# Kernel tuning notes

Measured on AMD Instinct MI355X. Metric: run time of the kernel, lower is better.

Reference implementation:

```python
import jax, jax.numpy as jnp
import numpy as np

DIM = 1024
B, S = 4, 2048


def setup_inputs() -> dict:
    key = jax.random.key(0)
    kx, kq, kk, kv, ko = jax.random.split(key, 5)
    scale = 1.0 / np.sqrt(DIM)
    return {
        "x": jax.random.normal(kx, (B, S, DIM), dtype=jnp.float32),
        "wq": jax.random.normal(kq, (DIM, DIM), dtype=jnp.float32) * scale,
        "wk": jax.random.normal(kk, (DIM, DIM), dtype=jnp.float32) * scale,
        "wv": jax.random.normal(kv, (DIM, DIM), dtype=jnp.float32) * scale,
        "wo": jax.random.normal(ko, (DIM, DIM), dtype=jnp.float32) * scale,
    }


def reference(x, wq, wk, wv, wo):
    # nn.Linear(y) = y @ W.T ; weights stored [out, in]
    q = jnp.einsum("bsd,ed->bse", x, wq)
    k = jnp.einsum("bsd,ed->bse", x, wk)
    v = jnp.einsum("bsd,ed->bse", x, wv)
    # NOTE: no head split in original module; full-dim attention, scale = sqrt(dim)
    scores = jnp.einsum("bqd,bkd->bqk", q, k) / jnp.sqrt(jnp.float32(DIM))
    attn = jax.nn.softmax(scores, axis=-1)
    ctx = jnp.einsum("bqk,bkd->bqd", attn, v)
    return jnp.einsum("bsd,ed->bse", ctx, wo)
```

## Files before the change

### kernel.cpp

```cpp
#include <hip/hip_runtime.h>
#include <hip/hip_bf16.h>
#include <cstdio>
#include <cstdint>


typedef __attribute__((ext_vector_type(8))) short short8;
typedef __attribute__((ext_vector_type(4))) float f32x4;

#define AS1(p) ((const __attribute__((address_space(1))) void*)(p))
#define AS3(p) ((__attribute__((address_space(3))) void*)(p))

__device__ __forceinline__ unsigned short f2bf(float f) {
  union { float f; uint32_t u; } c; c.f = f;
  uint32_t u = c.u + 0x7fffu + ((c.u >> 16) & 1u);
  return (unsigned short)(u >> 16);
}

__global__ void cvt_f32_bf16(const float* __restrict__ in,
                             unsigned short* __restrict__ out, int n4) {
  int i = blockIdx.x * 256 + threadIdx.x;
  if (i >= n4) return;
  float4 v = ((const float4*)in)[i];
  ushort4 o;
  o.x = f2bf(v.x); o.y = f2bf(v.y); o.z = f2bf(v.z); o.w = f2bf(v.w);
  ((ushort4*)out)[i] = o;
}

__global__ void transpose_bf16(const unsigned short* __restrict__ V,
                               unsigned short* __restrict__ Vt) {
  __shared__ unsigned short tile[64][72];
  const int b = blockIdx.z;
  const unsigned short* v = V + (size_t)b * 2048 * 1024;
  unsigned short* vt = Vt + (size_t)b * 1024 * 2048;
  const int d0 = blockIdx.x * 64, s0 = blockIdx.y * 64;
  const int t = threadIdx.x;
#pragma unroll
  for (int it = 0; it < 16; ++it) {
    int idx = it * 256 + t, r = idx >> 6, c = idx & 63;
    tile[r][c] = v[(size_t)(s0 + r) * 1024 + d0 + c];
  }
  __syncthreads();
#pragma unroll
  for (int it = 0; it < 16; ++it) {
    int idx = it * 256 + t, r = idx >> 6, c = idx & 63;
    vt[(size_t)(d0 + r) * 2048 + s0 + c] = tile[c][r];
  }
}

__global__ void softmax_rows(const float* __restrict__ S,
                             unsigned short* __restrict__ P) {
  const size_t row = blockIdx.x;
  const float* s = S + row * 2048;
  const int t = threadIdx.x, l = t & 63, w = t >> 6;
  float4 v0 = ((const float4*)s)[t * 2];
  float4 v1 = ((const float4*)s)[t * 2 + 1];
  float x[8] = {v0.x, v0.y, v0.z, v0.w, v1.x, v1.y, v1.z, v1.w};
  float m = x[0];
#pragma unroll
  for (int j = 1; j < 8; ++j) m = fmaxf(m, x[j]);
#pragma unroll
  for (int d = 32; d; d >>= 1) m = fmaxf(m, __shfl_xor(m, d));
  __shared__ float rm[4], rs[4];
  if (l == 0) rm[w] = m;
  __syncthreads();
  m = fmaxf(fmaxf(rm[0], rm[1]), fmaxf(rm[2], rm[3]));
  float e[8], sum = 0.f;
#pragma unroll
  for (int j = 0; j < 8; ++j) { e[j] = __expf(x[j] - m); sum += e[j]; }
#pragma unroll
  for (int d = 32; d; d >>= 1) sum += __shfl_xor(sum, d);
  if (l == 0) rs[w] = sum;
  __syncthreads();
  float inv = 1.0f / (rs[0] + rs[1] + rs[2] + rs[3]);
  short8 o;
#pragma unroll
  for (int j = 0; j < 8; ++j) o[j] = (short)f2bf(e[j] * inv);
  *(short8*)(P + row * 2048 + t * 8) = o;
}

__device__ __forceinline__ void store_out(float* p, float v) { *p = v; }
__device__ __forceinline__ void store_out(unsigned short* p, float v) { *p = f2bf(v); }

template <typename OutT>
__global__ __launch_bounds__(256, 2) void gemm_bt(
    const unsigned short* __restrict__ A, const unsigned short* __restrict__ B,
    OutT* __restrict__ C, int lda, int ldb, int ldc, int kIters,
    long long aStride, long long bStride, long long cStride, float scale) {
  __shared__ unsigned short ldsA[4096];
  __shared__ unsigned short ldsB[4096];
  const int t = threadIdx.x, l = t & 63, w = t >> 6;
  const int wr = w >> 1, wc = w & 1;
  const int r0 = blockIdx.y * 128, c0 = blockIdx.x * 128;
  A += (size_t)blockIdx.z * aStride;
  B += (size_t)blockIdx.z * bStride;
  C += (size_t)blockIdx.z * cStride;

  const unsigned short* aP = A + (size_t)(r0 + w * 16 + (l & 15)) * lda + (l >> 4) * 8;
  const unsigned short* bP = B + (size_t)(c0 + w * 16 + (l & 15)) * ldb + (l >> 4) * 8;
  const size_t a64 = (size_t)64 * lda, b64 = (size_t)64 * ldb;
  unsigned short* dA1 = &ldsA[w * 512];
  unsigned short* dA2 = &ldsA[2048 + w * 512];
  unsigned short* dB1 = &ldsB[w * 512];
  unsigned short* dB2 = &ldsB[2048 + w * 512];

  f32x4 acc[4][4] = {};

  for (int kt = 0; kt < kIters; ++kt) {
    __builtin_amdgcn_global_load_lds(AS1(aP),       AS3(dA1), 16, 0, 0);
    __builtin_amdgcn_global_load_lds(AS1(aP + a64), AS3(dA2), 16, 0, 0);
    __builtin_amdgcn_global_load_lds(AS1(bP),       AS3(dB1), 16, 0, 0);
    __builtin_amdgcn_global_load_lds(AS1(bP + b64), AS3(dB2), 16, 0, 0);
    aP += 32; bP += 32;
    __syncthreads();
    short8 af[4], bfv[4];
#pragma unroll
    for (int m = 0; m < 4; ++m)
      af[m] = *(const short8*)&ldsA[(wr * 4 + m) * 512 + l * 8];
#pragma unroll
    for (int n = 0; n < 4; ++n)
      bfv[n] = *(const short8*)&ldsB[(wc * 4 + n) * 512 + l * 8];
#pragma unroll
    for (int m = 0; m < 4; ++m)
#pragma unroll
      for (int n = 0; n < 4; ++n)
        acc[m][n] = __builtin_amdgcn_mfma_f32_16x16x32_bf16(af[m], bfv[n], acc[m][n], 0, 0, 0);
    __syncthreads();
  }

  const int cr = (l >> 4) * 4, cc = l & 15;
#pragma unroll
  for (int m = 0; m < 4; ++m)
#pragma unroll
    for (int n = 0; n < 4; ++n) {
      int col = c0 + wc * 64 + n * 16 + cc;
#pragma unroll
      for (int i = 0; i < 4; ++i) {
        int row = r0 + wr * 64 + m * 16 + cr + i;
        store_out(&C[(size_t)row * ldc + col], acc[m][n][i] * scale);
      }
    }
}

static const size_t OFF_XB  = 0;
static const size_t OFF_WQ  = 16777216;
static const size_t OFF_WK  = 18874368;
static const size_t OFF_WV  = 20971520;
static const size_t OFF_WO  = 23068672;
static const size_t OFF_Q   = 25165824;
static const size_t OFF_K   = 41943040;
static const size_t OFF_V   = 58720256;
static const size_t OFF_VT  = 75497472;
static const size_t OFF_SC  = 92274688;
static const size_t OFF_P   = 159383552;
static const size_t OFF_CTX = 192937984;
static const size_t WS_NEED = 209715200;

extern "C" void kernel_launch(void* const* d_in, const int* in_sizes, int n_in,
                              void* d_out, int out_size, void* d_ws, size_t ws_size,
                              hipStream_t stream) {
  const float* x  = (const float*)d_in[0];
  const float* wq = (const float*)d_in[1];
  const float* wk = (const float*)d_in[2];
  const float* wv = (const float*)d_in[3];
  const float* wo = (const float*)d_in[4];
  float* out = (float*)d_out;

  if (ws_size < WS_NEED) {
    fprintf(stderr, "kernel_launch: ws_size=%zu < needed %zu\n", ws_size, WS_NEED);
    return;
  }
  char* ws = (char*)d_ws;
  unsigned short* xb  = (unsigned short*)(ws + OFF_XB);
  unsigned short* wqb = (unsigned short*)(ws + OFF_WQ);
  unsigned short* wkb = (unsigned short*)(ws + OFF_WK);
  unsigned short* wvb = (unsigned short*)(ws + OFF_WV);
  unsigned short* wob = (unsigned short*)(ws + OFF_WO);
  unsigned short* Qb  = (unsigned short*)(ws + OFF_Q);
  unsigned short* Kb  = (unsigned short*)(ws + OFF_K);
  unsigned short* Vb  = (unsigned short*)(ws + OFF_V);
  unsigned short* Vt  = (unsigned short*)(ws + OFF_VT);
  float*          Sc  = (float*)(ws + OFF_SC);
  unsigned short* Pb  = (unsigned short*)(ws + OFF_P);
  unsigned short* Cx  = (unsigned short*)(ws + OFF_CTX);

  cvt_f32_bf16<<<8192, 256, 0, stream>>>(x,  xb,  2097152);
  cvt_f32_bf16<<<1024, 256, 0, stream>>>(wq, wqb, 262144);
  cvt_f32_bf16<<<1024, 256, 0, stream>>>(wk, wkb, 262144);
  cvt_f32_bf16<<<1024, 256, 0, stream>>>(wv, wvb, 262144);
  cvt_f32_bf16<<<1024, 256, 0, stream>>>(wo, wob, 262144);

  gemm_bt<unsigned short><<<dim3(8, 64, 1), 256, 0, stream>>>(
      xb, wqb, Qb, 1024, 1024, 1024, 32, 0, 0, 0, 1.0f);
  gemm_bt<unsigned short><<<dim3(8, 64, 1), 256, 0, stream>>>(
      xb, wkb, Kb, 1024, 1024, 1024, 32, 0, 0, 0, 1.0f);
  gemm_bt<unsigned short><<<dim3(8, 64, 1), 256, 0, stream>>>(
      xb, wvb, Vb, 1024, 1024, 1024, 32, 0, 0, 0, 1.0f);

  transpose_bf16<<<dim3(16, 32, 4), 256, 0, stream>>>(Vb, Vt);

  gemm_bt<float><<<dim3(16, 16, 4), 256, 0, stream>>>(
      Qb, Kb, Sc, 1024, 1024, 2048, 32,
      2097152LL, 2097152LL, 4194304LL, 0.03125f);

  softmax_rows<<<8192, 256, 0, stream>>>(Sc, Pb);

  gemm_bt<unsigned short><<<dim3(8, 16, 4), 256, 0, stream>>>(
      Pb, Vt, Cx, 2048, 2048, 1024, 64,
      4194304LL, 2097152LL, 2097152LL, 1.0f);

  gemm_bt<float><<<dim3(8, 64, 1), 256, 0, stream>>>(
      Cx, wob, out, 1024, 1024, 1024, 32, 0, 0, 0, 1.0f);
}
```

Before: 419.2 us.

## Pipeline GEMM with 4-stage LDS ring, 8 waves, XCD swizzle, batched launches

Rewrites the bf16 GEMM to use 512 threads (8 waves, each owning a 32x64 sub-tile), a 4-deep LDS ring buffer prefetched two k-steps ahead with explicit vmcnt waits, and a single barrier per iteration. It also remaps workgroup IDs so consecutive tiles land on the same XCD for L2 reuse. The four weight conversions are merged into one launch, and the Q/K/V projections into one batched GEMM via a z-stride. The intent is to hide global-load latency and cut launch overhead, at the cost of more LDS (64 KB) and register pressure, plus reliance on a barrier-reuse pattern that has to be correct with 4 buffers.

```diff
diff --git a/kernel.cpp b/kernel.cpp
--- a/kernel.cpp
+++ b/kernel.cpp
@@ -24,6 +24,18 @@
   ushort4 o;
   o.x = f2bf(v.x); o.y = f2bf(v.y); o.z = f2bf(v.z); o.w = f2bf(v.w);
   ((ushort4*)out)[i] = o;
+}
+
+__global__ void cvt_w4(const float* __restrict__ a, const float* __restrict__ b,
+                       const float* __restrict__ c, const float* __restrict__ d,
+                       unsigned short* __restrict__ out) {
+  const float* s = (blockIdx.y == 0) ? a : (blockIdx.y == 1) ? b
+                 : (blockIdx.y == 2) ? c : d;
+  int i = blockIdx.x * 256 + threadIdx.x;
+  float4 v = ((const float4*)s)[i];
+  ushort4 o;
+  o.x = f2bf(v.x); o.y = f2bf(v.y); o.z = f2bf(v.z); o.w = f2bf(v.w);
+  ((ushort4*)(out + (size_t)blockIdx.y * 1048576))[i] = o;
 }
 
 __global__ void transpose_bf16(const unsigned short* __restrict__ V,
@@ -82,60 +94,86 @@
 __device__ __forceinline__ void store_out(unsigned short* p, float v) { *p = f2bf(v); }
 
 template <typename OutT>
-__global__ __launch_bounds__(256, 2) void gemm_bt(
+__global__ __launch_bounds__(512, 4) void gemm_bt(
     const unsigned short* __restrict__ A, const unsigned short* __restrict__ B,
-    OutT* __restrict__ C, int lda, int ldb, int ldc, int kIters,
+    OutT* __restrict__ C, int lda, int ldb, int ldc, int nk,
     long long aStride, long long bStride, long long cStride, float scale) {
-  __shared__ unsigned short ldsA[4096];
-  __shared__ unsigned short ldsB[4096];
+  __shared__ unsigned short lds[32768];
   const int t = threadIdx.x, l = t & 63, w = t >> 6;
   const int wr = w >> 1, wc = w & 1;
-  const int r0 = blockIdx.y * 128, c0 = blockIdx.x * 128;
-  A += (size_t)blockIdx.z * aStride;
-  B += (size_t)blockIdx.z * bStride;
-  C += (size_t)blockIdx.z * cStride;
-
-  const unsigned short* aP = A + (size_t)(r0 + w * 16 + (l & 15)) * lda + (l >> 4) * 8;
-  const unsigned short* bP = B + (size_t)(c0 + w * 16 + (l & 15)) * ldb + (l >> 4) * 8;
-  const size_t a64 = (size_t)64 * lda, b64 = (size_t)64 * ldb;
-  unsigned short* dA1 = &ldsA[w * 512];
-  unsigned short* dA2 = &ldsA[2048 + w * 512];
-  unsigned short* dB1 = &ldsB[w * 512];
-  unsigned short* dB2 = &ldsB[2048 + w * 512];
-
-  f32x4 acc[4][4] = {};
-
-  for (int kt = 0; kt < kIters; ++kt) {
-    __builtin_amdgcn_global_load_lds(AS1(aP),       AS3(dA1), 16, 0, 0);
-    __builtin_amdgcn_global_load_lds(AS1(aP + a64), AS3(dA2), 16, 0, 0);
-    __builtin_amdgcn_global_load_lds(AS1(bP),       AS3(dB1), 16, 0, 0);
-    __builtin_amdgcn_global_load_lds(AS1(bP + b64), AS3(dB2), 16, 0, 0);
-    aP += 32; bP += 32;
-    __syncthreads();
-    short8 af[4], bfv[4];
-#pragma unroll
-    for (int m = 0; m < 4; ++m)
-      af[m] = *(const short8*)&ldsA[(wr * 4 + m) * 512 + l * 8];
+
+  const int gx = gridDim.x, gy = gridDim.y;
+  int f = blockIdx.x + gx * (blockIdx.y + gy * blockIdx.z);
+  int nwg = gx * gy * gridDim.z;
+  int work = ((nwg & 7) == 0) ? ((f & 7) * (nwg >> 3) + (f >> 3)) : f;
+  const int bx = work % gx;
+  int rem = work / gx;
+  const int by = rem % gy, bz = rem / gy;
+  const int r0 = by * 128, col0 = bx * 128;
+  A += (size_t)bz * aStride;
+  B += (size_t)bz * bStride;
+  C += (size_t)bz * cStride;
+
+  const unsigned short* sp[2];
+  int dstoff[2];
+#pragma unroll
+  for (int j = 0; j < 2; ++j) {
+    int c = 2 * w + j;
+    bool isA = c < 8;
+    int row = (isA ? r0 + c * 16 : col0 + (c - 8) * 16) + (l & 15);
+    sp[j] = (isA ? A : B) + (size_t)row * (isA ? lda : ldb) + (l >> 4) * 8;
+    dstoff[j] = c * 1024;
+  }
+
+#define STAGE(kt_, b_)                                                        \
+  do {                                                                        \
+    _Pragma("unroll") for (int j = 0; j < 2; ++j)                             \
+        __builtin_amdgcn_global_load_lds(AS1(sp[j] + (size_t)(kt_) * 32),     \
+                                         AS3((char*)lds + (b_) * 16384 + dstoff[j]), \
+                                         16, 0, 0);                           \
+  } while (0)
+
+  f32x4 acc[2][4] = {};
+  STAGE(0, 0);
+  if (nk > 1) STAGE(1, 1);
+
+  for (int kt = 0; kt < nk; ++kt) {
+    if (kt + 2 < nk) {
+      STAGE(kt + 2, (kt + 2) & 3);
+      asm volatile("s_waitcnt vmcnt(4)" ::: "memory");
+    } else if (kt + 1 < nk) {
+      asm volatile("s_waitcnt vmcnt(2)" ::: "memory");
+    } else {
+      asm volatile("s_waitcnt vmcnt(0)" ::: "memory");
+    }
+    __builtin_amdgcn_s_barrier();
+    asm volatile("" ::: "memory");
+
+    const int bb = (kt & 3) * 8192;
+    short8 af[2], bfv[4];
+#pragma unroll
+    for (int m = 0; m < 2; ++m)
+      af[m] = *(const short8*)&lds[bb + ((wr * 2 + m) * 64 + l) * 8];
 #pragma unroll
     for (int n = 0; n < 4; ++n)
-      bfv[n] = *(const short8*)&ldsB[(wc * 4 + n) * 512 + l * 8];
-#pragma unroll
-    for (int m = 0; m < 4; ++m)
+      bfv[n] = *(const short8*)&lds[bb + 4096 + ((wc * 4 + n) * 64 + l) * 8];
+#pragma unroll
+    for (int m = 0; m < 2; ++m)
 #pragma unroll
       for (int n = 0; n < 4; ++n)
         acc[m][n] = __builtin_amdgcn_mfma_f32_16x16x32_bf16(af[m], bfv[n], acc[m][n], 0, 0, 0);
-    __syncthreads();
-  }
+  }
+#undef STAGE
 
   const int cr = (l >> 4) * 4, cc = l & 15;
 #pragma unroll
-  for (int m = 0; m < 4; ++m)
+  for (int m = 0; m < 2; ++m)
 #pragma unroll
     for (int n = 0; n < 4; ++n) {
-      int col = c0 + wc * 64 + n * 16 + cc;
+      int col = col0 + wc * 64 + n * 16 + cc;
 #pragma unroll
       for (int i = 0; i < 4; ++i) {
-        int row = r0 + wr * 64 + m * 16 + cr + i;
+        int row = r0 + wr * 32 + m * 16 + cr + i;
         store_out(&C[(size_t)row * ldc + col], acc[m][n][i] * scale);
       }
     }
@@ -172,9 +210,6 @@
   char* ws = (char*)d_ws;
   unsigned short* xb  = (unsigned short*)(ws + OFF_XB);
   unsigned short* wqb = (unsigned short*)(ws + OFF_WQ);
-  unsigned short* wkb = (unsigned short*)(ws + OFF_WK);
-  unsigned short* wvb = (unsigned short*)(ws + OFF_WV);
-  unsigned short* wob = (unsigned short*)(ws + OFF_WO);
   unsigned short* Qb  = (unsigned short*)(ws + OFF_Q);
   unsigned short* Kb  = (unsigned short*)(ws + OFF_K);
   unsigned short* Vb  = (unsigned short*)(ws + OFF_V);
@@ -182,32 +217,26 @@
   float*          Sc  = (float*)(ws + OFF_SC);
   unsigned short* Pb  = (unsigned short*)(ws + OFF_P);
   unsigned short* Cx  = (unsigned short*)(ws + OFF_CTX);
-
-  cvt_f32_bf16<<<8192, 256, 0, stream>>>(x,  xb,  2097152);
-  cvt_f32_bf16<<<1024, 256, 0, stream>>>(wq, wqb, 262144);
-  cvt_f32_bf16<<<1024, 256, 0, stream>>>(wk, wkb, 262144);
-  cvt_f32_bf16<<<1024, 256, 0, stream>>>(wv, wvb, 262144);
-  cvt_f32_bf16<<<1024, 256, 0, stream>>>(wo, wob, 262144);
-
-  gemm_bt<unsigned short><<<dim3(8, 64, 1), 256, 0, stream>>>(
-      xb, wqb, Qb, 1024, 1024, 1024, 32, 0, 0, 0, 1.0f);
-  gemm_bt<unsigned short><<<dim3(8, 64, 1), 256, 0, stream>>>(
-      xb, wkb, Kb, 1024, 1024, 1024, 32, 0, 0, 0, 1.0f);
-  gemm_bt<unsigned short><<<dim3(8, 64, 1), 256, 0, stream>>>(
-      xb, wvb, Vb, 1024, 1024, 1024, 32, 0, 0, 0, 1.0f);
+  unsigned short* wob = (unsigned short*)(ws + OFF_WO);
+
+  cvt_f32_bf16<<<8192, 256, 0, stream>>>(x, xb, 2097152);
+  cvt_w4<<<dim3(1024, 4, 1), 256, 0, stream>>>(wq, wk, wv, wo, wqb);
+
+  gemm_bt<unsigned short><<<dim3(8, 64, 3), 512, 0, stream>>>(
+      xb, wqb, Qb, 1024, 1024, 1024, 32, 0, 1048576LL, 8388608LL, 1.0f);
 
   transpose_bf16<<<dim3(16, 32, 4), 256, 0, stream>>>(Vb, Vt);
 
-  gemm_bt<float><<<dim3(16, 16, 4), 256, 0, stream>>>(
+  gemm_bt<float><<<dim3(16, 16, 4), 512, 0, stream>>>(
       Qb, Kb, Sc, 1024, 1024, 2048, 32,
       2097152LL, 2097152LL, 4194304LL, 0.03125f);
 
   softmax_rows<<<8192, 256, 0, stream>>>(Sc, Pb);
 
-  gemm_bt<unsigned short><<<dim3(8, 16, 4), 256, 0, stream>>>(
+  gemm_bt<unsigned short><<<dim3(8, 16, 4), 512, 0, stream>>>(
       Pb, Vt, Cx, 2048, 2048, 1024, 64,
       4194304LL, 2097152LL, 2097152LL, 1.0f);
 
-  gemm_bt<float><<<dim3(8, 64, 1), 256, 0, stream>>>(
+  gemm_bt<float><<<dim3(8, 64, 1), 512, 0, stream>>>(
       Cx, wob, out, 1024, 1024, 1024, 32, 0, 0, 0, 1.0f);
 }
```

Result: faster. 376.8 us (-10.1%).
